# Performance work log

Hardware: AMD Instinct MI355X
Metric: run time of the kernel (lower is better)

The kernel has to match this reference:

```python
import jax, jax.numpy as jnp
import numpy as np

B, S, D, ENC_S = 4, 1024, 1024, 512
DI, DFF, DFE = 2048, 4096, 2048
NA, NB, E, H = 2, 6, 8, 16
TOP_K = 2


def setup_inputs():
    key = jax.random.key(0)
    ks = jax.random.split(key, 24)
    s = 0.02
    n = jax.random.normal
    return {
        "x": n(ks[0], (B, S, D), jnp.float32),
        "encoder_out": n(ks[1], (B, ENC_S, D), jnp.float32),
        "encoder_mask": jnp.ones((B, ENC_S), dtype=bool),
        "padding_mask": jnp.ones((B, S), dtype=bool),
        "encoder_available": jax.random.randint(ks[2], (B,), 0, 2, jnp.int32),
        "ln_g": jnp.ones((D,), jnp.float32),
        "ln_b": jnp.zeros((D,), jnp.float32),
        "ssm_Win": s * n(ks[3], (D, 2 * DI), jnp.float32),
        "ssm_a": n(ks[4], (DI,), jnp.float32),
        "ssm_Wout": s * n(ks[5], (DI, D), jnp.float32),
        "attn_Wqkv": s * n(ks[6], (D, 3 * D), jnp.float32),
        "attn_Wo": s * n(ks[7], (D, D), jnp.float32),
        "beta_ssm": 0.8 * jnp.ones((D,), jnp.float32),
        "beta_attn": 0.2 * jnp.ones((D,), jnp.float32),
        "se_W1": s * n(ks[8], (D, DFF), jnp.float32),
        "se_b1": jnp.zeros((DFF,), jnp.float32),
        "se_W2": s * n(ks[9], (DFF, D), jnp.float32),
        "se_b2": jnp.zeros((D,), jnp.float32),
        "r_W": s * n(ks[10], (D + 1, E), jnp.float32),
        "r_b": jnp.zeros((E,), jnp.float32),
        "ea_Wq": s * n(ks[11], (NA, D, D), jnp.float32),
        "ea_Wk": s * n(ks[12], (NA, D, D), jnp.float32),
        "ea_Wv": s * n(ks[13], (NA, D, D), jnp.float32),
        "ea_Wo": s * n(ks[14], (NA, D, D), jnp.float32),
        "ea_W1": s * n(ks[15], (NA, D, DFE), jnp.float32),
        "ea_W2": s * n(ks[16], (NA, DFE, D), jnp.float32),
        "eb_W1": s * n(ks[17], (NB, D, DFE), jnp.float32),
        "eb_W2": s * n(ks[18], (NB, DFE, D), jnp.float32),
    }


def _moe_forward(x, encoder_out, ln_g, ln_b, ssm_Win, ssm_a, ssm_Wout,
                 attn_Wqkv, attn_Wo, beta_ssm, beta_attn,
                 se_W1, se_b1, se_W2, se_b2, r_W, r_b,
                 ea_Wq, ea_Wk, ea_Wv, ea_Wo, ea_W1, ea_W2, eb_W1, eb_W2,
                 encoder_mask, padding_mask, encoder_available):
    # ---- Hymba fusion: LayerNorm -> SSM + causal attention, per-channel mix ----
    mu = x.mean(-1, keepdims=True)
    var = ((x - mu) ** 2).mean(-1, keepdims=True)
    h = (x - mu) * jax.lax.rsqrt(var + 1e-5) * ln_g + ln_b

    # SSM pathway: gated diagonal linear recurrence h_t = a*h_{t-1} + (1-a)*u_t
    u = h @ ssm_Win                       # (B,S,2*DI)
    z, xs = jnp.split(u, 2, axis=-1)
    a = jax.nn.sigmoid(ssm_a)             # (DI,)
    a_full = jnp.broadcast_to(a, xs.shape)
    b_in = (1.0 - a) * xs

    def comb(c1, c2):
        a1, b1 = c1
        a2, b2 = c2
        return a1 * a2, a2 * b1 + b2

    hs = jax.lax.associative_scan(comb, (a_full, b_in), axis=1)[1]
    ssm_out = (hs * jax.nn.silu(z)) @ ssm_Wout   # (B,S,D)

    # Attention pathway: causal MHA with key padding mask
    dh = D // H
    qkv = h @ attn_Wqkv
    q, k, v = jnp.split(qkv, 3, axis=-1)
    sp = lambda t: t.reshape(B, S, H, dh).transpose(0, 2, 1, 3)  # (B,H,S,dh)
    q, k, v = sp(q), sp(k), sp(v)
    scores = jnp.einsum('bhqd,bhkd->bhqk', q, k) / np.sqrt(dh).astype(np.float32)
    causal = jnp.tril(jnp.ones((S, S), dtype=bool))
    keymask = padding_mask[:, None, None, :]
    scores = jnp.where(causal[None, None] & keymask, scores, -1e9)
    p = jax.nn.softmax(scores, axis=-1)
    ao = jnp.einsum('bhqk,bhkd->bhqd', p, v).transpose(0, 2, 1, 3).reshape(B, S, D)
    attn_out = ao @ attn_Wo

    x = x + beta_ssm * ssm_out + beta_attn * attn_out  # residual after fusion

    # ---- MoE ----
    N = B * S
    x_flat = x.reshape(N, D)
    enc_avail_tok = jnp.repeat(encoder_available.astype(x.dtype), S)[:, None]  # (N,1)

    shared_delta = jax.nn.gelu(x_flat @ se_W1 + se_b1) @ se_W2 + se_b2

    # Router: top-k gating over softmax(logits)
    logits = jnp.concatenate([x_flat, enc_avail_tok], axis=-1) @ r_W + r_b  # (N,E)
    probs = jax.nn.softmax(logits, axis=-1)
    topv, topi = jax.lax.top_k(probs, TOP_K)
    gates = jnp.zeros_like(probs).at[jnp.arange(N)[:, None], topi].set(topv)
    gates = gates / (gates.sum(-1, keepdims=True) + 1e-9)

    # Hard S-mode gate: zero type-A experts where encoder unavailable, renormalize
    s_mode = enc_avail_tok == 0                       # (N,1)
    type_a = jnp.arange(E) < NA                       # (E,)
    gates = jnp.where(s_mode & type_a[None, :], 0.0, gates)
    gates = gates / (gates.sum(-1, keepdims=True) + 1e-6)

    # Type-A experts: per-token cross-attention to own batch's encoder, then FFN.
    # (dense over tokens; zero gates kill inactive tokens -> same math as sparse dispatch)
    qA = jnp.einsum('bsd,edf->ebsf', x, ea_Wq)
    kA = jnp.einsum('bmd,edf->ebmf', encoder_out, ea_Wk)
    vA = jnp.einsum('bmd,edf->ebmf', encoder_out, ea_Wv)
    sA = jnp.einsum('ebsf,ebmf->ebsm', qA, kA) / np.sqrt(D).astype(np.float32)
    sA = jnp.where(encoder_mask[None, :, None, :], sA, -1e9)
    pA = jax.nn.softmax(sA, axis=-1)
    ctx = jnp.einsum('ebsm,ebmf->ebsf', pA, vA)
    hA = x[None] + jnp.einsum('ebsf,efd->ebsd', ctx, ea_Wo)
    outA = jnp.einsum('ebsh,ehd->ebsd',
                      jax.nn.gelu(jnp.einsum('ebsd,edh->ebsh', hA, ea_W1)), ea_W2)
    outA = outA.reshape(NA, N, D)

    # Type-B experts: plain FFN on tokens
    outB = jnp.einsum('enh,ehd->end',
                      jax.nn.gelu(jnp.einsum('nd,edh->enh', x_flat, eb_W1)), eb_W2)

    out_all = jnp.concatenate([outA, outB], axis=0)   # (E,N,D)
    routed_delta = jnp.einsum('ne,end->nd', gates, out_all)

    return x + (shared_delta + routed_delta).reshape(B, S, D)


def reference(x, encoder_out, encoder_mask, padding_mask, encoder_available,
              ln_g, ln_b, ssm_Win, ssm_a, ssm_Wout, attn_Wqkv, attn_Wo,
              beta_ssm, beta_attn, se_W1, se_b1, se_W2, se_b2, r_W, r_b,
              ea_Wq, ea_Wk, ea_Wv, ea_Wo, ea_W1, ea_W2, eb_W1, eb_W2):
    return _moe_forward(x, encoder_out, ln_g, ln_b, ssm_Win, ssm_a, ssm_Wout,
                        attn_Wqkv, attn_Wo, beta_ssm, beta_attn,
                        se_W1, se_b1, se_W2, se_b2, r_W, r_b,
                        ea_Wq, ea_Wk, ea_Wv, ea_Wo, ea_W1, ea_W2, eb_W1, eb_W2,
                        encoder_mask, padding_mask, encoder_available)
```

## Files before the change

kernel.cpp:

```cpp
#include <hip/hip_runtime.h>
#include <hip/hip_bf16.h>
#include <math.h>

#define BB 4
#define SS 1024
#define DD 1024
#define ENCS 512
#define DI 2048
#define DFF 4096
#define DFE 2048
#define NA 2
#define NB 6
#define NE 8
#define NH 16
#define NTOK (BB*SS)
#define W1SZ ((long)DD*DFE)

typedef unsigned short u16;
typedef __bf16 bfrag __attribute__((ext_vector_type(8)));
typedef float  ffrag __attribute__((ext_vector_type(4)));

__device__ __forceinline__ float gelu_f(float x) {
    const float c = 0.7978845608028654f;
    float t = tanhf(c * (x + 0.044715f * x * x * x));
    return 0.5f * x * (1.f + t);
}

__device__ __forceinline__ u16 f2bf(float f) {
    unsigned u = __float_as_uint(f);
    u += 0x7fffu + ((u >> 16) & 1u);
    return (u16)(u >> 16);
}

__device__ __forceinline__ void split_bf(float v, u16& hi, u16& lo) {
    hi = f2bf(v);
    float hf = __uint_as_float((unsigned)hi << 16);
    lo = f2bf(v - hf);
}

typedef const __attribute__((address_space(1))) unsigned int* gas_t;
typedef __attribute__((address_space(3))) unsigned int* las_t;
__device__ __forceinline__ void gload16(const u16* g, u16* l) {
    __builtin_amdgcn_global_load_lds((gas_t)g, (las_t)l, 16, 0, 0);
}

__device__ __forceinline__ int flds(int row, int p) {
    return row * 64 + (((p ^ (row & 7)) & 7) << 3);
}

__global__ __launch_bounds__(256) void gemm_mfma(
    const u16* __restrict__ A, const u16* __restrict__ Bt,
    float* __restrict__ Cf, u16* __restrict__ Ch,
    int M, int N, int K,
    long sAb, long sBb, long sCb,
    const float* __restrict__ bias, const float* __restrict__ res,
    const float* __restrict__ rowscale, int rs_stride,
    int accum, int do_gelu)
{
    __shared__ u16 As[3][4096];
    __shared__ u16 Bs[3][4096];
    const int tid = threadIdx.x;
    const int w = tid >> 6, l = tid & 63;
    const int wm = w >> 1, wn = w & 1;
    const int bz = blockIdx.z;
    A  += (long)bz * sAb;
    Bt += (long)bz * sBb;
    const int m0 = blockIdx.y * 128, n0 = blockIdx.x * 128;

    const int c0 = 2 * w, c1 = c0 + 1;
    const int rl0 = c0 * 16 + (l >> 2), rl1 = c1 * 16 + (l >> 2);
    const int p = l & 3;
    const int gb0 = p ^ ((rl0 ^ (rl0 >> 2)) & 3);
    const int gb1 = p ^ ((rl1 ^ (rl1 >> 2)) & 3);
    const u16* gA0 = A  + (long)(m0 + rl0) * K + gb0 * 8;
    const u16* gA1 = A  + (long)(m0 + rl1) * K + gb1 * 8;
    const u16* gB0 = Bt + (long)(n0 + rl0) * K + gb0 * 8;
    const u16* gB1 = Bt + (long)(n0 + rl1) * K + gb1 * 8;
    const int d0 = c0 * 512, d1 = c1 * 512;

    const int q = l >> 4, fr = l & 15;
    int offA[4], offB[4];
    #pragma unroll
    for (int t = 0; t < 4; t++) {
        int ra = wm * 64 + t * 16 + fr;
        offA[t] = ra * 32 + (q ^ ((ra ^ (ra >> 2)) & 3)) * 8;
        int rb = wn * 64 + t * 16 + fr;
        offB[t] = rb * 32 + (q ^ ((rb ^ (rb >> 2)) & 3)) * 8;
    }

    ffrag acc[16];
    #pragma unroll
    for (int i = 0; i < 16; i++) acc[i] = (ffrag){0.f, 0.f, 0.f, 0.f};

    const int nsteps = K >> 5;
    #define STAGE1(bi, k0) do { \
        gload16(gA0 + (k0), &As[bi][d0]); \
        gload16(gA1 + (k0), &As[bi][d1]); \
        gload16(gB0 + (k0), &Bs[bi][d0]); \
        gload16(gB1 + (k0), &Bs[bi][d1]); } while (0)

    STAGE1(0, 0);
    STAGE1(1, 32);
    int cur = 0;
    for (int t = 0; t < nsteps; ++t) {
        int rem = nsteps - 1 - t;
        if (rem >= 2) {
            int nb = cur + 2; if (nb >= 3) nb -= 3;
            STAGE1(nb, (t + 2) << 5);
            asm volatile("s_waitcnt vmcnt(8)" ::: "memory");
        } else if (rem == 1) {
            asm volatile("s_waitcnt vmcnt(4)" ::: "memory");
        } else {
            asm volatile("s_waitcnt vmcnt(0)" ::: "memory");
        }
        __builtin_amdgcn_s_barrier();
        bfrag af[4], bf[4];
        #pragma unroll
        for (int i = 0; i < 4; i++) {
            af[i] = *(const bfrag*)(&As[cur][0] + offA[i]);
            bf[i] = *(const bfrag*)(&Bs[cur][0] + offB[i]);
        }
        #pragma unroll
        for (int mt = 0; mt < 4; mt++)
            #pragma unroll
            for (int nt = 0; nt < 4; nt++)
                acc[mt * 4 + nt] = __builtin_amdgcn_mfma_f32_16x16x32_bf16(
                    af[mt], bf[nt], acc[mt * 4 + nt], 0, 0, 0);
        __builtin_amdgcn_s_barrier();
        cur = (cur == 2) ? 0 : cur + 1;
    }
    #undef STAGE1

    const long cbase = (long)bz * sCb;
    #pragma unroll
    for (int mt = 0; mt < 4; mt++) {
        #pragma unroll
        for (int nt = 0; nt < 4; nt++) {
            ffrag v = acc[mt * 4 + nt];
            int col = n0 + wn * 64 + nt * 16 + fr;
            int row0 = m0 + wm * 64 + mt * 16 + q * 4;
            float bv = bias ? bias[col] : 0.f;
            #pragma unroll
            for (int j = 0; j < 4; j++) {
                int row = row0 + j;
                float x = v[j] + bv;
                if (do_gelu) x = gelu_f(x);
                if (rowscale) x *= rowscale[(long)row * rs_stride];
                long idx = cbase + (long)row * N + col;
                if (res) x += res[(long)row * N + col];
                if (accum) { Cf[idx] += x; }
                else {
                    if (Cf) Cf[idx] = x;
                    if (Ch) Ch[idx] = f2bf(x);
                }
            }
        }
    }
}

__global__ __launch_bounds__(256) void gemm3_mfma(
    const u16* __restrict__ Ahi, const u16* __restrict__ Alo,
    const u16* __restrict__ Bhi, const u16* __restrict__ Blo,
    float* __restrict__ Cf, int M, int N, int K)
{
    __shared__ u16 Ah[2][4096];
    __shared__ u16 Al[2][4096];
    __shared__ u16 Bh[2][4096];
    __shared__ u16 Bl[2][4096];
    const int tid = threadIdx.x;
    const int w = tid >> 6, l = tid & 63;
    const int wm = w >> 1, wn = w & 1;
    const int m0 = blockIdx.y * 128, n0 = blockIdx.x * 128;

    const int c0 = 2 * w, c1 = c0 + 1;
    const int rl0 = c0 * 16 + (l >> 2), rl1 = c1 * 16 + (l >> 2);
    const int p = l & 3;
    const int gb0 = p ^ ((rl0 ^ (rl0 >> 2)) & 3);
    const int gb1 = p ^ ((rl1 ^ (rl1 >> 2)) & 3);
    const long oa0 = (long)(m0 + rl0) * K + gb0 * 8;
    const long oa1 = (long)(m0 + rl1) * K + gb1 * 8;
    const long ob0 = (long)(n0 + rl0) * K + gb0 * 8;
    const long ob1 = (long)(n0 + rl1) * K + gb1 * 8;
    const u16* gAh0 = Ahi + oa0; const u16* gAh1 = Ahi + oa1;
    const u16* gAl0 = Alo + oa0; const u16* gAl1 = Alo + oa1;
    const u16* gBh0 = Bhi + ob0; const u16* gBh1 = Bhi + ob1;
    const u16* gBl0 = Blo + ob0; const u16* gBl1 = Blo + ob1;
    const int d0 = c0 * 512, d1 = c1 * 512;

    const int q = l >> 4, fr = l & 15;
    int offA[4], offB[4];
    #pragma unroll
    for (int t = 0; t < 4; t++) {
        int ra = wm * 64 + t * 16 + fr;
        offA[t] = ra * 32 + (q ^ ((ra ^ (ra >> 2)) & 3)) * 8;
        int rb = wn * 64 + t * 16 + fr;
        offB[t] = rb * 32 + (q ^ ((rb ^ (rb >> 2)) & 3)) * 8;
    }

    ffrag acc[16];
    #pragma unroll
    for (int i = 0; i < 16; i++) acc[i] = (ffrag){0.f, 0.f, 0.f, 0.f};

    const int nsteps = K >> 5;
    #define STAGE3(bi, k0) do { \
        gload16(gAh0 + (k0), &Ah[bi][d0]); \
        gload16(gAh1 + (k0), &Ah[bi][d1]); \
        gload16(gAl0 + (k0), &Al[bi][d0]); \
        gload16(gAl1 + (k0), &Al[bi][d1]); \
        gload16(gBh0 + (k0), &Bh[bi][d0]); \
        gload16(gBh1 + (k0), &Bh[bi][d1]); \
        gload16(gBl0 + (k0), &Bl[bi][d0]); \
        gload16(gBl1 + (k0), &Bl[bi][d1]); } while (0)

    int cur = 0;
    STAGE3(0, 0);
    for (int t = 0; t < nsteps; ++t) {
        if (t + 1 < nsteps) {
            STAGE3(cur ^ 1, (t + 1) << 5);
            asm volatile("s_waitcnt vmcnt(8)" ::: "memory");
        } else {
            asm volatile("s_waitcnt vmcnt(0)" ::: "memory");
        }
        __builtin_amdgcn_s_barrier();
        bfrag ah[4], al[4], bh[4], bl[4];
        #pragma unroll
        for (int i = 0; i < 4; i++) {
            ah[i] = *(const bfrag*)(&Ah[cur][0] + offA[i]);
            al[i] = *(const bfrag*)(&Al[cur][0] + offA[i]);
            bh[i] = *(const bfrag*)(&Bh[cur][0] + offB[i]);
            bl[i] = *(const bfrag*)(&Bl[cur][0] + offB[i]);
        }
        #pragma unroll
        for (int mt = 0; mt < 4; mt++) {
            #pragma unroll
            for (int nt = 0; nt < 4; nt++) {
                ffrag a = acc[mt * 4 + nt];
                a = __builtin_amdgcn_mfma_f32_16x16x32_bf16(ah[mt], bh[nt], a, 0, 0, 0);
                a = __builtin_amdgcn_mfma_f32_16x16x32_bf16(ah[mt], bl[nt], a, 0, 0, 0);
                a = __builtin_amdgcn_mfma_f32_16x16x32_bf16(al[mt], bh[nt], a, 0, 0, 0);
                acc[mt * 4 + nt] = a;
            }
        }
        __builtin_amdgcn_s_barrier();
        cur ^= 1;
    }
    #undef STAGE3

    #pragma unroll
    for (int mt = 0; mt < 4; mt++) {
        #pragma unroll
        for (int nt = 0; nt < 4; nt++) {
            ffrag v = acc[mt * 4 + nt];
            int col = n0 + wn * 64 + nt * 16 + fr;
            int row0 = m0 + wm * 64 + mt * 16 + q * 4;
            #pragma unroll
            for (int j = 0; j < 4; j++)
                Cf[(long)(row0 + j) * N + col] = v[j];
        }
    }
}

static inline void ggemm(hipStream_t st, const u16* A, const u16* Bt,
    float* Cf, u16* Ch, int M, int N, int K, int batch,
    long sA, long sB, long sC,
    const float* bias, const float* res, const float* rs, int rss,
    int accum, int gelu)
{
    dim3 g(N / 128, M / 128, batch), b(256);
    gemm_mfma<<<g, b, 0, st>>>(A, Bt, Cf, Ch, M, N, K, sA, sB, sC,
                               bias, res, rs, rss, accum, gelu);
}

static inline void ggemm3(hipStream_t st, const u16* Ahi, const u16* Alo,
    const u16* Bhi, const u16* Blo, float* Cf, int M, int N, int K)
{
    dim3 g(N / 128, M / 128, 1), b(256);
    gemm3_mfma<<<g, b, 0, st>>>(Ahi, Alo, Bhi, Blo, Cf, M, N, K);
}

__global__ __launch_bounds__(256) void moe_w1(
    const u16* __restrict__ Xa, const u16* __restrict__ Xb,
    const u16* __restrict__ W1a, const u16* __restrict__ W1b,
    u16* __restrict__ ffp,
    const int* __restrict__ idxAll, const int* __restrict__ cntAll,
    const int* __restrict__ offAll, int N, int K)
{
    const int z = blockIdx.z;
    const int m0 = blockIdx.y * 128;
    if (m0 >= cntAll[z]) return;
    const int* idx = idxAll + z * NTOK;
    const u16* X  = (z < NA) ? (Xa + (long)z * NTOK * DD) : Xb;
    const u16* Wt = (z < 4) ? (W1a + (long)z * W1SZ) : (W1b + (long)(z - 4) * W1SZ);
    u16* ff = ffp + (long)offAll[z] * N;

    __shared__ u16 As[3][4096];
    __shared__ u16 Bs[3][4096];
    const int tid = threadIdx.x;
    const int w = tid >> 6, l = tid & 63;
    const int wm = w >> 1, wn = w & 1;
    const int n0 = blockIdx.x * 128;
    const int c0 = 2 * w, c1 = c0 + 1;
    const int rl0 = c0 * 16 + (l >> 2), rl1 = c1 * 16 + (l >> 2);
    const int p = l & 3;
    const int gb0 = p ^ ((rl0 ^ (rl0 >> 2)) & 3);
    const int gb1 = p ^ ((rl1 ^ (rl1 >> 2)) & 3);
    const int t0 = idx[m0 + rl0], t1 = idx[m0 + rl1];
    const u16* gA0 = X + (long)t0 * K + gb0 * 8;
    const u16* gA1 = X + (long)t1 * K + gb1 * 8;
    const u16* gB0 = Wt + (long)(n0 + rl0) * K + gb0 * 8;
    const u16* gB1 = Wt + (long)(n0 + rl1) * K + gb1 * 8;
    const int d0 = c0 * 512, d1 = c1 * 512;
    const int q = l >> 4, fr = l & 15;
    int offA[4], offB[4];
    #pragma unroll
    for (int t = 0; t < 4; t++) {
        int ra = wm * 64 + t * 16 + fr;
        offA[t] = ra * 32 + (q ^ ((ra ^ (ra >> 2)) & 3)) * 8;
        int rb = wn * 64 + t * 16 + fr;
        offB[t] = rb * 32 + (q ^ ((rb ^ (rb >> 2)) & 3)) * 8;
    }
    ffrag acc[16];
    #pragma unroll
    for (int i = 0; i < 16; i++) acc[i] = (ffrag){0.f, 0.f, 0.f, 0.f};

    const int nsteps = K >> 5;
    #define STAGEM(bi, k0) do { \
        gload16(gA0 + (k0), &As[bi][d0]); \
        gload16(gA1 + (k0), &As[bi][d1]); \
        gload16(gB0 + (k0), &Bs[bi][d0]); \
        gload16(gB1 + (k0), &Bs[bi][d1]); } while (0)

    STAGEM(0, 0);
    STAGEM(1, 32);
    int cur = 0;
    for (int t = 0; t < nsteps; ++t) {
        int rem = nsteps - 1 - t;
        if (rem >= 2) {
            int nb = cur + 2; if (nb >= 3) nb -= 3;
            STAGEM(nb, (t + 2) << 5);
            asm volatile("s_waitcnt vmcnt(8)" ::: "memory");
        } else if (rem == 1) {
            asm volatile("s_waitcnt vmcnt(4)" ::: "memory");
        } else {
            asm volatile("s_waitcnt vmcnt(0)" ::: "memory");
        }
        __builtin_amdgcn_s_barrier();
        bfrag af[4], bf[4];
        #pragma unroll
        for (int i = 0; i < 4; i++) {
            af[i] = *(const bfrag*)(&As[cur][0] + offA[i]);
            bf[i] = *(const bfrag*)(&Bs[cur][0] + offB[i]);
        }
        #pragma unroll
        for (int mt = 0; mt < 4; mt++)
            #pragma unroll
            for (int nt = 0; nt < 4; nt++)
                acc[mt * 4 + nt] = __builtin_amdgcn_mfma_f32_16x16x32_bf16(
                    af[mt], bf[nt], acc[mt * 4 + nt], 0, 0, 0);
        __builtin_amdgcn_s_barrier();
        cur = (cur == 2) ? 0 : cur + 1;
    }
    #undef STAGEM

    #pragma unroll
    for (int mt = 0; mt < 4; mt++)
        #pragma unroll
        for (int nt = 0; nt < 4; nt++) {
            ffrag v = acc[mt * 4 + nt];
            int col = n0 + wn * 64 + nt * 16 + fr;
            int row0 = m0 + wm * 64 + mt * 16 + q * 4;
            #pragma unroll
            for (int j = 0; j < 4; j++)
                ff[(long)(row0 + j) * N + col] = f2bf(gelu_f(v[j]));
        }
}

__global__ __launch_bounds__(256) void moe_w2(
    const u16* __restrict__ ffp,
    const u16* __restrict__ W2a, const u16* __restrict__ W2b,
    float* __restrict__ out,
    const int* __restrict__ idxAll, const float* __restrict__ gvAll,
    const int* __restrict__ cntAll, const int* __restrict__ offAll,
    int N, int K)
{
    const int z = blockIdx.z;
    const int cnt = cntAll[z];
    const int m0 = blockIdx.y * 128;
    if (m0 >= cnt) return;
    const int* idx = idxAll + z * NTOK;
    const float* gval = gvAll + z * NTOK;
    const u16* Aseg = ffp + (long)offAll[z] * K;
    const u16* Wt = (z < 4) ? (W2a + (long)z * W1SZ) : (W2b + (long)(z - 4) * W1SZ);

    __shared__ u16 As[3][4096];
    __shared__ u16 Bs[3][4096];
    const int tid = threadIdx.x;
    const int w = tid >> 6, l = tid & 63;
    const int wm = w >> 1, wn = w & 1;
    const int n0 = blockIdx.x * 128;
    const int c0 = 2 * w, c1 = c0 + 1;
    const int rl0 = c0 * 16 + (l >> 2), rl1 = c1 * 16 + (l >> 2);
    const int p = l & 3;
    const int gb0 = p ^ ((rl0 ^ (rl0 >> 2)) & 3);
    const int gb1 = p ^ ((rl1 ^ (rl1 >> 2)) & 3);
    const u16* gA0 = Aseg + (long)(m0 + rl0) * K + gb0 * 8;
    const u16* gA1 = Aseg + (long)(m0 + rl1) * K + gb1 * 8;
    const u16* gB0 = Wt + (long)(n0 + rl0) * K + gb0 * 8;
    const u16* gB1 = Wt + (long)(n0 + rl1) * K + gb1 * 8;
    const int d0 = c0 * 512, d1 = c1 * 512;
    const int q = l >> 4, fr = l & 15;
    int offA[4], offB[4];
    #pragma unroll
    for (int t = 0; t < 4; t++) {
        int ra = wm * 64 + t * 16 + fr;
        offA[t] = ra * 32 + (q ^ ((ra ^ (ra >> 2)) & 3)) * 8;
        int rb = wn * 64 + t * 16 + fr;
        offB[t] = rb * 32 + (q ^ ((rb ^ (rb >> 2)) & 3)) * 8;
    }
    ffrag acc[16];
    #pragma unroll
    for (int i = 0; i < 16; i++) acc[i] = (ffrag){0.f, 0.f, 0.f, 0.f};

    const int nsteps = K >> 5;
    #define STAGEW(bi, k0) do { \
        gload16(gA0 + (k0), &As[bi][d0]); \
        gload16(gA1 + (k0), &As[bi][d1]); \
        gload16(gB0 + (k0), &Bs[bi][d0]); \
        gload16(gB1 + (k0), &Bs[bi][d1]); } while (0)

    STAGEW(0, 0);
    STAGEW(1, 32);
    int cur = 0;
    for (int t = 0; t < nsteps; ++t) {
        int rem = nsteps - 1 - t;
        if (rem >= 2) {
            int nb = cur + 2; if (nb >= 3) nb -= 3;
            STAGEW(nb, (t + 2) << 5);
            asm volatile("s_waitcnt vmcnt(8)" ::: "memory");
        } else if (rem == 1) {
            asm volatile("s_waitcnt vmcnt(4)" ::: "memory");
        } else {
            asm volatile("s_waitcnt vmcnt(0)" ::: "memory");
        }
        __builtin_amdgcn_s_barrier();
        bfrag af[4], bf[4];
        #pragma unroll
        for (int i = 0; i < 4; i++) {
            af[i] = *(const bfrag*)(&As[cur][0] + offA[i]);
            bf[i] = *(const bfrag*)(&Bs[cur][0] + offB[i]);
        }
        #pragma unroll
        for (int mt = 0; mt < 4; mt++)
            #pragma unroll
            for (int nt = 0; nt < 4; nt++)
                acc[mt * 4 + nt] = __builtin_amdgcn_mfma_f32_16x16x32_bf16(
                    af[mt], bf[nt], acc[mt * 4 + nt], 0, 0, 0);
        __builtin_amdgcn_s_barrier();
        cur = (cur == 2) ? 0 : cur + 1;
    }
    #undef STAGEW

    #pragma unroll
    for (int mt = 0; mt < 4; mt++)
        #pragma unroll
        for (int nt = 0; nt < 4; nt++) {
            ffrag v = acc[mt * 4 + nt];
            int col = n0 + wn * 64 + nt * 16 + fr;
            int row0 = m0 + wm * 64 + mt * 16 + q * 4;
            #pragma unroll
            for (int j = 0; j < 4; j++) {
                int m = row0 + j;
                if (m < cnt)
                    atomicAdd(&out[(long)idx[m] * N + col], gval[m] * v[j]);
            }
        }
}

__global__ __launch_bounds__(256) void moe_zero(int* __restrict__ idx, int* __restrict__ cnt)
{
    int i = blockIdx.x * 256 + threadIdx.x;
    if (i < NE * NTOK) idx[i] = 0;
    if (i < NE) cnt[i] = 0;
}

__global__ __launch_bounds__(256) void moe_build(
    const float* __restrict__ gates, int* __restrict__ idx,
    float* __restrict__ gval, int* __restrict__ cnt)
{
    int t = blockIdx.x * 256 + threadIdx.x;
    #pragma unroll
    for (int e = 0; e < NE; e++) {
        float g = gates[(long)t * NE + e];
        if (g > 0.f) {
            int ppos = atomicAdd(&cnt[e], 1);
            idx[e * NTOK + ppos] = t;
            gval[e * NTOK + ppos] = g;
        }
    }
}

__global__ __launch_bounds__(64) void moe_off(
    const int* __restrict__ cnt, int* __restrict__ off)
{
    if (threadIdx.x == 0) {
        int o = 0;
        for (int e = 0; e < NE; e++) { off[e] = o; o += (cnt[e] + 127) & ~127; }
    }
}

__global__ __launch_bounds__(256) void convT_kernel(
    const float* __restrict__ src, u16* __restrict__ dst, int K, int N,
    long sS, long sD)
{
    __shared__ float t[32][33];
    src += (long)blockIdx.z * sS;
    dst += (long)blockIdx.z * sD;
    int n0 = blockIdx.x * 32, k0 = blockIdx.y * 32;
    int tx = threadIdx.x & 31, ty = threadIdx.x >> 5;
    #pragma unroll
    for (int j = 0; j < 4; j++)
        t[ty + j * 8][tx] = src[(long)(k0 + ty + j * 8) * N + n0 + tx];
    __syncthreads();
    #pragma unroll
    for (int j = 0; j < 4; j++)
        dst[(long)(n0 + ty + j * 8) * K + k0 + tx] = f2bf(t[tx][ty + j * 8]);
}

__global__ __launch_bounds__(256) void convT2_kernel(
    const float* __restrict__ src, u16* __restrict__ dhi, u16* __restrict__ dlo,
    int K, int N)
{
    __shared__ float t[32][33];
    int n0 = blockIdx.x * 32, k0 = blockIdx.y * 32;
    int tx = threadIdx.x & 31, ty = threadIdx.x >> 5;
    #pragma unroll
    for (int j = 0; j < 4; j++)
        t[ty + j * 8][tx] = src[(long)(k0 + ty + j * 8) * N + n0 + tx];
    __syncthreads();
    #pragma unroll
    for (int j = 0; j < 4; j++) {
        float v = t[tx][ty + j * 8];
        u16 hi, lo; split_bf(v, hi, lo);
        long o = (long)(n0 + ty + j * 8) * K + k0 + tx;
        dhi[o] = hi; dlo[o] = lo;
    }
}

__global__ __launch_bounds__(256) void conv_kernel(
    const float* __restrict__ s, u16* __restrict__ d)
{
    int i = (blockIdx.x * 256 + threadIdx.x) * 4;
    float4 v = *(const float4*)(s + i);
    ushort4 o;
    o.x = f2bf(v.x); o.y = f2bf(v.y); o.z = f2bf(v.z); o.w = f2bf(v.w);
    *(ushort4*)(d + i) = o;
}

__global__ __launch_bounds__(256) void ln_kernel(
    const float* __restrict__ x, const float* __restrict__ g,
    const float* __restrict__ b, u16* __restrict__ hhi, u16* __restrict__ hlo)
{
    int token = blockIdx.x;
    int tid = threadIdx.x;
    const float* xr = x + (long)token * DD;
    float4 xv = *(const float4*)(xr + tid * 4);
    float s  = xv.x + xv.y + xv.z + xv.w;
    float sq = xv.x*xv.x + xv.y*xv.y + xv.z*xv.z + xv.w*xv.w;
    #pragma unroll
    for (int off = 32; off; off >>= 1) {
        s  += __shfl_xor(s, off);
        sq += __shfl_xor(sq, off);
    }
    __shared__ float ws[4], wq[4];
    int wid = tid >> 6, lane = tid & 63;
    if (lane == 0) { ws[wid] = s; wq[wid] = sq; }
    __syncthreads();
    s  = ws[0] + ws[1] + ws[2] + ws[3];
    sq = wq[0] + wq[1] + wq[2] + wq[3];
    float mu  = s * (1.f / DD);
    float var = sq * (1.f / DD) - mu * mu;
    float inv = rsqrtf(var + 1e-5f);
    float4 gv = *(const float4*)(g + tid * 4);
    float4 bv = *(const float4*)(b + tid * 4);
    float o[4];
    o[0] = (xv.x - mu) * inv * gv.x + bv.x;
    o[1] = (xv.y - mu) * inv * gv.y + bv.y;
    o[2] = (xv.z - mu) * inv * gv.z + bv.z;
    o[3] = (xv.w - mu) * inv * gv.w + bv.w;
    ushort4 oh, ol;
    split_bf(o[0], oh.x, ol.x); split_bf(o[1], oh.y, ol.y);
    split_bf(o[2], oh.z, ol.z); split_bf(o[3], oh.w, ol.w);
    *(ushort4*)(hhi + (long)token * DD + tid * 4) = oh;
    *(ushort4*)(hlo + (long)token * DD + tid * 4) = ol;
}

__global__ __launch_bounds__(256) void scan_p1(
    const float* __restrict__ u, const float* __restrict__ ssma,
    float* __restrict__ part)
{
    int i = blockIdx.x * 256 + threadIdx.x;
    int c = i & 2047, ch = (i >> 11) & 7, b = i >> 14;
    float a = 1.f / (1.f + expf(-ssma[c])), om = 1.f - a;
    const float* ux = u + (long)b * SS * (2 * DI) + DI + c;
    float h = 0.f;
    int t0 = ch * 128;
    #pragma unroll 4
    for (int t = t0; t < t0 + 128; ++t) h = a * h + om * ux[(long)t * (2 * DI)];
    part[i] = h;
}

__global__ __launch_bounds__(256) void scan_p2(
    const float* __restrict__ ssma, const float* __restrict__ part,
    float* __restrict__ init)
{
    int j = blockIdx.x * 256 + threadIdx.x;
    int c = j & 2047, b = j >> 11;
    float a = 1.f / (1.f + expf(-ssma[c]));
    float ap = a;
    #pragma unroll
    for (int i = 0; i < 7; i++) ap *= ap;
    float carry = 0.f;
    int base = b * 16384 + c;
    #pragma unroll
    for (int ch = 0; ch < 8; ch++) {
        init[base + ch * 2048] = carry;
        carry = ap * carry + part[base + ch * 2048];
    }
}

__global__ __launch_bounds__(256) void scan_p3(
    const float* __restrict__ u, const float* __restrict__ ssma,
    const float* __restrict__ init,
    u16* __restrict__ ihi, u16* __restrict__ ilo)
{
    int i = blockIdx.x * 256 + threadIdx.x;
    int c = i & 2047, ch = (i >> 11) & 7, b = i >> 14;
    float a = 1.f / (1.f + expf(-ssma[c])), om = 1.f - a;
    const float* uz = u + (long)b * SS * (2 * DI) + c;
    long obase = (long)b * SS * DI + c;
    float h = init[i];
    int t0 = ch * 128;
    #pragma unroll 2
    for (int t = t0; t < t0 + 128; ++t) {
        float z  = uz[(long)t * (2 * DI)];
        float xv = uz[(long)t * (2 * DI) + DI];
        h = a * h + om * xv;
        float sz = z / (1.f + expf(-z));
        u16 hi, lo; split_bf(h * sz, hi, lo);
        ihi[obase + (long)t * DI] = hi;
        ilo[obase + (long)t * DI] = lo;
    }
}

__global__ __launch_bounds__(256) void qk_prep(
    const float* __restrict__ qkv,
    u16* __restrict__ Qhi, u16* __restrict__ Qlo,
    u16* __restrict__ Khi, u16* __restrict__ Klo)
{
    int tok = blockIdx.x * 4 + (threadIdx.x >> 6);
    int l = threadIdx.x & 63;
    int b = tok >> 10, s = tok & 1023;
    const float* src = qkv + (long)tok * 3072;
    #pragma unroll
    for (int h = 0; h < 16; h++) {
        long dst = ((long)(b * 16 + h) * 1024 + s) * 64 + l;
        u16 hi, lo;
        split_bf(src[h * 64 + l], hi, lo);
        Qhi[dst] = hi; Qlo[dst] = lo;
        split_bf(src[1024 + h * 64 + l], hi, lo);
        Khi[dst] = hi; Klo[dst] = lo;
    }
}

__global__ __launch_bounds__(256) void v_prep(
    const float* __restrict__ qkv, u16* __restrict__ Vthi, u16* __restrict__ Vtlo)
{
    __shared__ float t[64][65];
    int st = blockIdx.x, bh = blockIdx.y;
    int b = bh >> 4, h = bh & 15;
    int tid = threadIdx.x;
    #pragma unroll
    for (int i = 0; i < 16; i++) {
        int e = tid + i * 256;
        int sl = e >> 6, d = e & 63;
        t[sl][d] = qkv[((long)(b * 1024 + st * 64 + sl)) * 3072 + 2048 + h * 64 + d];
    }
    __syncthreads();
    #pragma unroll
    for (int i = 0; i < 16; i++) {
        int e = tid + i * 256;
        int d = e >> 6, sl = e & 63;
        float v = t[sl][d];
        u16 hi, lo; split_bf(v, hi, lo);
        long o = ((long)bh * 64 + d) * 1024 + st * 64 + sl;
        Vthi[o] = hi; Vtlo[o] = lo;
    }
}

__global__ __launch_bounds__(256) void flash_mfma(
    const u16* __restrict__ Qhi, const u16* __restrict__ Qlo,
    const u16* __restrict__ Khi, const u16* __restrict__ Klo,
    const u16* __restrict__ Vthi, const u16* __restrict__ Vtlo,
    u16* __restrict__ aohi, u16* __restrict__ aolo)
{
    __shared__ u16 Qh[4096], Ql[4096], Kh[4096], Kl[4096], Vh[4096], Vl[4096];
    __shared__ u16 Ph[4][1024], Pl[4][1024];
    const int qt = (SS / 64 - 1) - blockIdx.x, bh = blockIdx.y;
    const int tid = threadIdx.x, w = tid >> 6, l = tid & 63;
    const int q0 = qt * 64;
    const int lr = l >> 3, ps = l & 7;
    const int cg = l & 15, quad = l >> 4;

    #pragma unroll
    for (int cc = 0; cc < 2; cc++) {
        int c = 2 * w + cc;
        int r = c * 8 + lr;
        int pl = ps ^ (r & 7);
        long gq = ((long)bh * 1024 + q0 + r) * 64 + pl * 8;
        long gk = ((long)bh * 1024 + r) * 64 + pl * 8;
        long gv = ((long)bh * 64 + r) * 1024 + pl * 8;
        gload16(Qhi + gq, Qh + c * 512 + l * 8);
        gload16(Qlo + gq, Ql + c * 512 + l * 8);
        gload16(Khi + gk, Kh + c * 512 + l * 8);
        gload16(Klo + gk, Kl + c * 512 + l * 8);
        gload16(Vthi + gv, Vh + c * 512 + l * 8);
        gload16(Vtlo + gv, Vl + c * 512 + l * 8);
    }
    __syncthreads();

    const int qrow = w * 16 + cg;
    const int offQ0 = flds(qrow, quad), offQ1 = flds(qrow, 4 + quad);
    bfrag qh0 = *(const bfrag*)(Qh + offQ0);
    bfrag qh1 = *(const bfrag*)(Qh + offQ1);
    bfrag ql0 = *(const bfrag*)(Ql + offQ0);
    bfrag ql1 = *(const bfrag*)(Ql + offQ1);

    ffrag O[4];
    #pragma unroll
    for (int i = 0; i < 4; i++) O[i] = (ffrag){0.f, 0.f, 0.f, 0.f};
    float mrun[4], lrun[4];
    #pragma unroll
    for (int j = 0; j < 4; j++) { mrun[j] = -1e30f; lrun[j] = 0.f; }

    for (int kt = 0; kt <= qt; kt++) {
        const bool pf = (kt < qt);
        uint4 rkh[2], rkl[2], rvh[2], rvl[2];
        if (pf) {
            int k0n = (kt + 1) * 64;
            #pragma unroll
            for (int cc = 0; cc < 2; cc++) {
                int c = 2 * w + cc;
                int r = c * 8 + lr;
                int pl = ps ^ (r & 7);
                long gk = ((long)bh * 1024 + k0n + r) * 64 + pl * 8;
                long gv = ((long)bh * 64 + r) * 1024 + k0n + pl * 8;
                rkh[cc] = *(const uint4*)(Khi + gk);
                rkl[cc] = *(const uint4*)(Klo + gk);
                rvh[cc] = *(const uint4*)(Vthi + gv);
                rvl[cc] = *(const uint4*)(Vtlo + gv);
            }
        }

        float s[4][4];
        #pragma unroll
        for (int nt = 0; nt < 4; nt++) {
            ffrag sc = (ffrag){0.f, 0.f, 0.f, 0.f};
            int kr = nt * 16 + cg;
            bfrag kh0 = *(const bfrag*)(Kh + flds(kr, quad));
            bfrag kh1 = *(const bfrag*)(Kh + flds(kr, 4 + quad));
            bfrag kl0 = *(const bfrag*)(Kl + flds(kr, quad));
            bfrag kl1 = *(const bfrag*)(Kl + flds(kr, 4 + quad));
            sc = __builtin_amdgcn_mfma_f32_16x16x32_bf16(qh0, kh0, sc, 0, 0, 0);
            sc = __builtin_amdgcn_mfma_f32_16x16x32_bf16(qh1, kh1, sc, 0, 0, 0);
            sc = __builtin_amdgcn_mfma_f32_16x16x32_bf16(qh0, kl0, sc, 0, 0, 0);
            sc = __builtin_amdgcn_mfma_f32_16x16x32_bf16(qh1, kl1, sc, 0, 0, 0);
            sc = __builtin_amdgcn_mfma_f32_16x16x32_bf16(ql0, kh0, sc, 0, 0, 0);
            sc = __builtin_amdgcn_mfma_f32_16x16x32_bf16(ql1, kh1, sc, 0, 0, 0);
            bool last = (kt == qt);
            #pragma unroll
            for (int j = 0; j < 4; j++) {
                float v = sc[j] * 0.125f;
                if (last && (nt * 16 + cg > w * 16 + quad * 4 + j)) v = -1e30f;
                s[nt][j] = v;
            }
        }
        #pragma unroll
        for (int j = 0; j < 4; j++) {
            float rm = fmaxf(fmaxf(s[0][j], s[1][j]), fmaxf(s[2][j], s[3][j]));
            rm = fmaxf(rm, __shfl_xor(rm, 1));
            rm = fmaxf(rm, __shfl_xor(rm, 2));
            rm = fmaxf(rm, __shfl_xor(rm, 4));
            rm = fmaxf(rm, __shfl_xor(rm, 8));
            float mn = fmaxf(mrun[j], rm);
            float alpha = __expf(mrun[j] - mn);
            float rs = 0.f;
            #pragma unroll
            for (int nt = 0; nt < 4; nt++) {
                float pv = __expf(s[nt][j] - mn);
                s[nt][j] = pv;
                rs += pv;
            }
            rs += __shfl_xor(rs, 1);
            rs += __shfl_xor(rs, 2);
            rs += __shfl_xor(rs, 4);
            rs += __shfl_xor(rs, 8);
            lrun[j] = lrun[j] * alpha + rs;
            mrun[j] = mn;
            #pragma unroll
            for (int ct = 0; ct < 4; ct++) O[ct][j] *= alpha;
        }
        #pragma unroll
        for (int nt = 0; nt < 4; nt++)
            #pragma unroll
            for (int j = 0; j < 4; j++) {
                int row = quad * 4 + j, col = nt * 16 + cg;
                int addr = row * 64 + (((col >> 3) ^ (row & 7)) << 3) + (col & 7);
                float pv = s[nt][j];
                u16 phv = f2bf(pv);
                float pf2 = __uint_as_float((unsigned)phv << 16);
                Ph[w][addr] = phv;
                Pl[w][addr] = f2bf(pv - pf2);
            }
        bfrag p0h = *(const bfrag*)(&Ph[w][0] + flds(cg, quad));
        bfrag p1h = *(const bfrag*)(&Ph[w][0] + flds(cg, 4 + quad));
        bfrag p0l = *(const bfrag*)(&Pl[w][0] + flds(cg, quad));
        bfrag p1l = *(const bfrag*)(&Pl[w][0] + flds(cg, 4 + quad));
        #pragma unroll
        for (int ct = 0; ct < 4; ct++) {
            int vr = ct * 16 + cg;
            bfrag vh0 = *(const bfrag*)(Vh + flds(vr, quad));
            bfrag vh1 = *(const bfrag*)(Vh + flds(vr, 4 + quad));
            bfrag vl0 = *(const bfrag*)(Vl + flds(vr, quad));
            bfrag vl1 = *(const bfrag*)(Vl + flds(vr, 4 + quad));
            O[ct] = __builtin_amdgcn_mfma_f32_16x16x32_bf16(p0h, vh0, O[ct], 0, 0, 0);
            O[ct] = __builtin_amdgcn_mfma_f32_16x16x32_bf16(p1h, vh1, O[ct], 0, 0, 0);
            O[ct] = __builtin_amdgcn_mfma_f32_16x16x32_bf16(p0h, vl0, O[ct], 0, 0, 0);
            O[ct] = __builtin_amdgcn_mfma_f32_16x16x32_bf16(p1h, vl1, O[ct], 0, 0, 0);
            O[ct] = __builtin_amdgcn_mfma_f32_16x16x32_bf16(p0l, vh0, O[ct], 0, 0, 0);
            O[ct] = __builtin_amdgcn_mfma_f32_16x16x32_bf16(p1l, vh1, O[ct], 0, 0, 0);
        }
        if (pf) {
            __syncthreads();
            #pragma unroll
            for (int cc = 0; cc < 2; cc++) {
                int c = 2 * w + cc;
                *(uint4*)(Kh + c * 512 + l * 8) = rkh[cc];
                *(uint4*)(Kl + c * 512 + l * 8) = rkl[cc];
                *(uint4*)(Vh + c * 512 + l * 8) = rvh[cc];
                *(uint4*)(Vl + c * 512 + l * 8) = rvl[cc];
            }
            __syncthreads();
        }
    }
    int b = bh >> 4, h = bh & 15;
    #pragma unroll
    for (int j = 0; j < 4; j++) {
        float inv = 1.f / lrun[j];
        int srow = q0 + w * 16 + quad * 4 + j;
        long base = ((long)(b * 1024 + srow)) * 1024 + h * 64 + cg;
        #pragma unroll
        for (int ct = 0; ct < 4; ct++) {
            float v = O[ct][j] * inv;
            u16 hi, lo; split_bf(v, hi, lo);
            aohi[base + ct * 16] = hi;
            aolo[base + ct * 16] = lo;
        }
    }
}

__global__ __launch_bounds__(256) void combine_kernel(
    const float* __restrict__ x, const float* __restrict__ ssm,
    const float* __restrict__ attn, const float* __restrict__ bs,
    const float* __restrict__ ba, float* __restrict__ x1, u16* __restrict__ x1h)
{
    int i = (blockIdx.x * 256 + threadIdx.x) * 4;
    int d = i & (DD - 1);
    float4 xv = *(const float4*)(x + i);
    float4 sv = *(const float4*)(ssm + i);
    float4 av = *(const float4*)(attn + i);
    float4 b1 = *(const float4*)(bs + d);
    float4 b2 = *(const float4*)(ba + d);
    float4 o;
    o.x = xv.x + b1.x * sv.x + b2.x * av.x;
    o.y = xv.y + b1.y * sv.y + b2.y * av.y;
    o.z = xv.z + b1.z * sv.z + b2.z * av.z;
    o.w = xv.w + b1.w * sv.w + b2.w * av.w;
    *(float4*)(x1 + i) = o;
    ushort4 oh;
    oh.x = f2bf(o.x); oh.y = f2bf(o.y); oh.z = f2bf(o.z); oh.w = f2bf(o.w);
    *(ushort4*)(x1h + i) = oh;
}

__global__ __launch_bounds__(256) void router_kernel(
    const float* __restrict__ x1, const int* __restrict__ enc_avail,
    const float* __restrict__ rW, const float* __restrict__ rb,
    float* __restrict__ gates)
{
    int token = blockIdx.x * 4 + (threadIdx.x >> 6);
    int lane = threadIdx.x & 63;
    int b = token >> 10;
    float acc[NE];
    #pragma unroll
    for (int e = 0; e < NE; e++) acc[e] = 0.f;
    const float* xrow = x1 + (long)token * DD;
    for (int d = lane; d < DD; d += 64) {
        float xv = xrow[d];
        const float* w = rW + (long)d * NE;
        #pragma unroll
        for (int e = 0; e < NE; e++) acc[e] += xv * w[e];
    }
    #pragma unroll
    for (int e = 0; e < NE; e++) {
        #pragma unroll
        for (int off = 32; off; off >>= 1) acc[e] += __shfl_xor(acc[e], off);
    }
    if (lane == 0) {
        int avail = enc_avail[b];
        float av = (float)avail;
        float lg[NE], pr[NE];
        #pragma unroll
        for (int e = 0; e < NE; e++) lg[e] = acc[e] + av * rW[(long)DD * NE + e] + rb[e];
        float mx = lg[0];
        #pragma unroll
        for (int e = 1; e < NE; e++) mx = fmaxf(mx, lg[e]);
        float sum = 0.f;
        #pragma unroll
        for (int e = 0; e < NE; e++) { pr[e] = expf(lg[e] - mx); sum += pr[e]; }
        float isum = 1.f / sum;
        #pragma unroll
        for (int e = 0; e < NE; e++) pr[e] *= isum;
        int i1 = 0;
        #pragma unroll
        for (int e = 1; e < NE; e++) if (pr[e] > pr[i1]) i1 = e;
        int i2 = (i1 == 0) ? 1 : 0;
        #pragma unroll
        for (int e = 0; e < NE; e++) if (e != i1 && pr[e] > pr[i2]) i2 = e;
        float g[NE];
        #pragma unroll
        for (int e = 0; e < NE; e++) g[e] = 0.f;
        g[i1] = pr[i1]; g[i2] = pr[i2];
        float s1 = g[i1] + g[i2] + 1e-9f;
        #pragma unroll
        for (int e = 0; e < NE; e++) g[e] /= s1;
        if (avail == 0) { g[0] = 0.f; g[1] = 0.f; }
        float s2 = 1e-6f;
        #pragma unroll
        for (int e = 0; e < NE; e++) s2 += g[e];
        float is2 = 1.f / s2;
        #pragma unroll
        for (int e = 0; e < NE; e++) gates[(long)token * NE + e] = g[e] * is2;
    }
}

__global__ __launch_bounds__(256) void softmax512_kernel(
    const float* __restrict__ sA, u16* __restrict__ pA, float scale)
{
    int row = blockIdx.x * 4 + (threadIdx.x >> 6);
    int lane = threadIdx.x & 63;
    const float* r = sA + (long)row * ENCS;
    u16* o = pA + (long)row * ENCS;
    float v[8];
    #pragma unroll
    for (int j = 0; j < 8; j++) v[j] = r[lane + j * 64] * scale;
    float mx = v[0];
    #pragma unroll
    for (int j = 1; j < 8; j++) mx = fmaxf(mx, v[j]);
    #pragma unroll
    for (int off = 32; off; off >>= 1) mx = fmaxf(mx, __shfl_xor(mx, off));
    float sum = 0.f;
    #pragma unroll
    for (int j = 0; j < 8; j++) { v[j] = __expf(v[j] - mx); sum += v[j]; }
    #pragma unroll
    for (int off = 32; off; off >>= 1) sum += __shfl_xor(sum, off);
    float inv = 1.f / sum;
    #pragma unroll
    for (int j = 0; j < 8; j++) o[lane + j * 64] = f2bf(v[j] * inv);
}

extern "C" void kernel_launch(void* const* d_in, const int* in_sizes, int n_in,
                              void* d_out, int out_size, void* d_ws, size_t ws_size,
                              hipStream_t stream) {
    const float* x    = (const float*)d_in[0];
    const float* enc  = (const float*)d_in[1];
    const int*   eav  = (const int*)d_in[4];
    const float* ln_g = (const float*)d_in[5];
    const float* ln_b = (const float*)d_in[6];
    const float* Win  = (const float*)d_in[7];
    const float* ssma = (const float*)d_in[8];
    const float* Wout = (const float*)d_in[9];
    const float* Wqkv = (const float*)d_in[10];
    const float* Wo   = (const float*)d_in[11];
    const float* bSsm = (const float*)d_in[12];
    const float* bAtt = (const float*)d_in[13];
    const float* seW1 = (const float*)d_in[14];
    const float* seb1 = (const float*)d_in[15];
    const float* seW2 = (const float*)d_in[16];
    const float* seb2 = (const float*)d_in[17];
    const float* rW   = (const float*)d_in[18];
    const float* rb   = (const float*)d_in[19];
    const float* eaWq = (const float*)d_in[20];
    const float* eaWk = (const float*)d_in[21];
    const float* eaWv = (const float*)d_in[22];
    const float* eaWo = (const float*)d_in[23];
    const float* eaW1 = (const float*)d_in[24];
    const float* eaW2 = (const float*)d_in[25];
    const float* ebW1 = (const float*)d_in[26];
    const float* ebW2 = (const float*)d_in[27];
    float* out = (float*)d_out;

    float* F = (float*)d_ws;
    float* f_big  = F;
    float* f_ssm  = F + 16777216;
    float* f_x1   = F + 20971520;
    float* f_part = F + 25165824;
    float* f_init = F + 25231360;
    float* f_gate = F + 25296896;
    u16* U = (u16*)(F + 25329664);
    u16* u_h_hi  = U;
    u16* u_h_lo  = U + 4194304;
    u16* u_in_hi = U + 8388608;
    u16* u_in_lo = U + 16777216;
    u16* u_ao_hi = U + 25165824;
    u16* u_ao_lo = U + 29360128;
    u16* u_wt    = U + 33554432;
    u16* u_wt_lo = U + 37748736;
    int*   moe_idx = (int*)(U + 41943040);
    float* moe_gv  = (float*)(moe_idx + NE * NTOK);
    int*   moe_cnt = (int*)(moe_gv + NE * NTOK);
    int*   moe_offp = moe_cnt + NE;

    float* f_u    = f_big;
    float* f_qkv  = f_big;
    float* f_attn = f_big + 12582912;
    u16*   u_ff   = (u16*)f_big;
    u16*   u_enc  = u_h_hi + 2097152;
    u16*   u_x1   = u_h_lo;
    u16* u_Qhi = u_h_hi, *u_Qlo = u_h_lo;
    u16* u_Khi = u_in_hi, *u_Klo = u_in_hi + 4194304;
    u16* u_Vthi = u_in_lo, *u_Vtlo = u_in_lo + 4194304;

    u16*   wq2   = u_wt;
    u16*   wk2   = u_wt_lo;
    u16*   wv2   = (u16*)f_ssm;
    u16*   wo2   = (u16*)f_ssm + 4194304;
    u16*   qA2   = u_ao_hi;
    u16*   kA2   = u_in_hi;
    u16*   vAt2  = u_in_hi + 4194304;
    float* sA2   = (float*)u_in_lo;
    u16*   ctx2  = u_in_lo;
    u16*   ffpool = (u16*)f_big;
    u16*   hA2   = (u16*)(f_big + 10485760);
    u16*   pA2   = (u16*)(f_big + 14680064);
    u16*   w1a   = u_ao_hi;
    u16*   w1b   = u_in_hi;
    u16*   w2a   = u_wt;
    u16*   w2b   = (u16*)f_ssm;

    #define CONVT(src, Kd, Nd)  convT_kernel <<<dim3((Nd)/32,(Kd)/32,1), dim3(256), 0, stream>>>(src, u_wt, Kd, Nd, 0, 0)
    #define CONVTB(src, dst, Kd, Nd, nb) convT_kernel<<<dim3((Nd)/32,(Kd)/32,(nb)), dim3(256), 0, stream>>>(src, dst, Kd, Nd, (long)(Kd)*(Nd), (long)(Kd)*(Nd))
    #define CONVT2(src, Kd, Nd) convT2_kernel<<<dim3((Nd)/32,(Kd)/32), dim3(256), 0, stream>>>(src, u_wt, u_wt_lo, Kd, Nd)

    ln_kernel<<<dim3(NTOK), dim3(256), 0, stream>>>(x, ln_g, ln_b, u_h_hi, u_h_lo);
    CONVT2(Win, DD, 2 * DI);
    ggemm3(stream, u_h_hi, u_h_lo, u_wt, u_wt_lo, f_u, NTOK, 2 * DI, DD);
    scan_p1<<<dim3(256), dim3(256), 0, stream>>>(f_u, ssma, f_part);
    scan_p2<<<dim3(32), dim3(256), 0, stream>>>(ssma, f_part, f_init);
    scan_p3<<<dim3(256), dim3(256), 0, stream>>>(f_u, ssma, f_init, u_in_hi, u_in_lo);
    CONVT2(Wout, DI, DD);
    ggemm3(stream, u_in_hi, u_in_lo, u_wt, u_wt_lo, f_ssm, NTOK, DD, DI);
    CONVT2(Wqkv, DD, 3 * DD);
    ggemm3(stream, u_h_hi, u_h_lo, u_wt, u_wt_lo, f_qkv, NTOK, 3 * DD, DD);
    qk_prep<<<dim3(NTOK / 4), dim3(256), 0, stream>>>(f_qkv, u_Qhi, u_Qlo, u_Khi, u_Klo);
    v_prep<<<dim3(SS / 64, BB * NH), dim3(256), 0, stream>>>(f_qkv, u_Vthi, u_Vtlo);
    flash_mfma<<<dim3(SS / 64, BB * NH), dim3(256), 0, stream>>>(
        u_Qhi, u_Qlo, u_Khi, u_Klo, u_Vthi, u_Vtlo, u_ao_hi, u_ao_lo);
    CONVT2(Wo, DD, DD);
    ggemm3(stream, u_ao_hi, u_ao_lo, u_wt, u_wt_lo, f_attn, NTOK, DD, DD);
    combine_kernel<<<dim3(NTOK * DD / 1024), dim3(256), 0, stream>>>(
        x, f_ssm, f_attn, bSsm, bAtt, f_x1, u_x1);
    router_kernel<<<dim3(NTOK / 4), dim3(256), 0, stream>>>(f_x1, eav, rW, rb, f_gate);
    moe_zero<<<dim3((NE * NTOK + 255) / 256), dim3(256), 0, stream>>>(moe_idx, moe_cnt);
    moe_build<<<dim3(NTOK / 256), dim3(256), 0, stream>>>(f_gate, moe_idx, moe_gv, moe_cnt);
    moe_off<<<dim3(1), dim3(64), 0, stream>>>(moe_cnt, moe_offp);
    CONVT(seW1, DD, DFF);
    ggemm(stream, u_x1, u_wt, nullptr, u_ff, NTOK, DFF, DD, 1, 0, 0, 0,
          seb1, nullptr, nullptr, 0, 0, 1);
    CONVT(seW2, DFF, DD);
    ggemm(stream, u_ff, u_wt, out, nullptr, NTOK, DD, DFF, 1, 0, 0, 0,
          seb2, f_x1, nullptr, 0, 0, 0);
    conv_kernel<<<dim3(BB * ENCS * DD / 1024), dim3(256), 0, stream>>>(enc, u_enc);

    CONVTB(eaWq, wq2, DD, DD, 2);
    CONVTB(eaWk, wk2, DD, DD, 2);
    CONVTB(eaWv, wv2, DD, DD, 2);
    CONVTB(eaWo, wo2, DD, DD, 2);
    ggemm(stream, u_x1, wq2, nullptr, qA2, NTOK, DD, DD, 2,
          0, (long)DD * DD, (long)NTOK * DD, nullptr, nullptr, nullptr, 0, 0, 0);
    ggemm(stream, u_enc, wk2, nullptr, kA2, BB * ENCS, DD, DD, 2,
          0, (long)DD * DD, (long)BB * ENCS * DD, nullptr, nullptr, nullptr, 0, 0, 0);
    for (int e = 0; e < NA; ++e)
        ggemm(stream, wv2 + (long)e * DD * DD, u_enc, nullptr,
              vAt2 + (long)e * 4 * DD * ENCS, DD, ENCS, DD, BB,
              0, (long)ENCS * DD, (long)DD * ENCS, nullptr, nullptr, nullptr, 0, 0, 0);
    ggemm(stream, qA2, kA2, sA2, nullptr, SS, ENCS, DD, 2 * BB,
          (long)SS * DD, (long)ENCS * DD, (long)SS * ENCS,
          nullptr, nullptr, nullptr, 0, 0, 0);
    softmax512_kernel<<<dim3(2 * NTOK / 4), dim3(256), 0, stream>>>(sA2, pA2, 0.03125f);
    ggemm(stream, pA2, vAt2, nullptr, ctx2, SS, DD, ENCS, 2 * BB,
          (long)SS * ENCS, (long)DD * ENCS, (long)SS * DD,
          nullptr, nullptr, nullptr, 0, 0, 0);
    ggemm(stream, ctx2, wo2, nullptr, hA2, NTOK, DD, DD, 2,
          (long)NTOK * DD, (long)DD * DD, (long)NTOK * DD,
          nullptr, f_x1, nullptr, 0, 0, 0);

    CONVTB(eaW1, w1a, DD, DFE, 2);
    CONVTB(ebW1, w1a + 2 * W1SZ, DD, DFE, 2);
    CONVTB(ebW1 + 2 * W1SZ, w1b, DD, DFE, 4);
    CONVTB(eaW2, w2a, DFE, DD, 2);
    CONVTB(ebW2, w2a + 2 * W1SZ, DFE, DD, 2);
    CONVTB(ebW2 + 2 * W1SZ, w2b, DFE, DD, 4);
    moe_w1<<<dim3(DFE / 128, NTOK / 128, NE), dim3(256), 0, stream>>>(
        hA2, u_x1, w1a, w1b, ffpool, moe_idx, moe_cnt, moe_offp, DFE, DD);
    moe_w2<<<dim3(DD / 128, NTOK / 128, NE), dim3(256), 0, stream>>>(
        ffpool, w2a, w2b, out, moe_idx, moe_gv, moe_cnt, moe_offp, DD, DFE);
    (void)in_sizes; (void)n_in; (void)out_size; (void)ws_size;
}
```

Baseline: 1.477 ms.

## Double-buffer K tiles and use direct global-to-LDS loads in flash attention

Replaces the register-staged K/V prefetch in the causal flash-attention kernel with direct global-to-LDS loads. K is double-buffered in shared memory, and V is loaded into its single buffer after the PV matmul, with manual vmcnt waits and raw s_barrier calls in place of __syncthreads. This removes register pressure and the extra LDS store pass, and lets K loads overlap compute. In exchange it adds 16 KB of LDS, which may lower occupancy, and it relies on careful manual waitcnt ordering, where a wrong count would be a correctness risk.

```diff
diff --git a/kernel.cpp b/kernel.cpp
--- a/kernel.cpp
+++ b/kernel.cpp
@@ -703,7 +703,9 @@
     const u16* __restrict__ Vthi, const u16* __restrict__ Vtlo,
     u16* __restrict__ aohi, u16* __restrict__ aolo)
 {
-    __shared__ u16 Qh[4096], Ql[4096], Kh[4096], Kl[4096], Vh[4096], Vl[4096];
+    __shared__ u16 Qh[4096], Ql[4096];
+    __shared__ u16 Kh[2][4096], Kl[2][4096];
+    __shared__ u16 Vh[4096], Vl[4096];
     __shared__ u16 Ph[4][1024], Pl[4][1024];
     const int qt = (SS / 64 - 1) - blockIdx.x, bh = blockIdx.y;
     const int tid = threadIdx.x, w = tid >> 6, l = tid & 63;
@@ -721,12 +723,13 @@
         long gv = ((long)bh * 64 + r) * 1024 + pl * 8;
         gload16(Qhi + gq, Qh + c * 512 + l * 8);
         gload16(Qlo + gq, Ql + c * 512 + l * 8);
-        gload16(Khi + gk, Kh + c * 512 + l * 8);
-        gload16(Klo + gk, Kl + c * 512 + l * 8);
+        gload16(Khi + gk, Kh[0] + c * 512 + l * 8);
+        gload16(Klo + gk, Kl[0] + c * 512 + l * 8);
         gload16(Vthi + gv, Vh + c * 512 + l * 8);
         gload16(Vtlo + gv, Vl + c * 512 + l * 8);
     }
-    __syncthreads();
+    asm volatile("s_waitcnt vmcnt(0)" ::: "memory");
+    __builtin_amdgcn_s_barrier();
 
     const int qrow = w * 16 + cg;
     const int offQ0 = flds(qrow, quad), offQ1 = flds(qrow, 4 + quad);
@@ -742,10 +745,9 @@
     #pragma unroll
     for (int j = 0; j < 4; j++) { mrun[j] = -1e30f; lrun[j] = 0.f; }
 
+    int cur = 0;
     for (int kt = 0; kt <= qt; kt++) {
-        const bool pf = (kt < qt);
-        uint4 rkh[2], rkl[2], rvh[2], rvl[2];
-        if (pf) {
+        if (kt < qt) {
             int k0n = (kt + 1) * 64;
             #pragma unroll
             for (int cc = 0; cc < 2; cc++) {
@@ -753,23 +755,26 @@
                 int r = c * 8 + lr;
                 int pl = ps ^ (r & 7);
                 long gk = ((long)bh * 1024 + k0n + r) * 64 + pl * 8;
-                long gv = ((long)bh * 64 + r) * 1024 + k0n + pl * 8;
-                rkh[cc] = *(const uint4*)(Khi + gk);
-                rkl[cc] = *(const uint4*)(Klo + gk);
-                rvh[cc] = *(const uint4*)(Vthi + gv);
-                rvl[cc] = *(const uint4*)(Vtlo + gv);
+                gload16(Khi + gk, Kh[cur ^ 1] + c * 512 + l * 8);
+                gload16(Klo + gk, Kl[cur ^ 1] + c * 512 + l * 8);
             }
-        }
-
+            asm volatile("s_waitcnt vmcnt(4)" ::: "memory");
+        } else {
+            asm volatile("s_waitcnt vmcnt(0)" ::: "memory");
+        }
+        __builtin_amdgcn_s_barrier();
+
+        const u16* KhC = Kh[cur];
+        const u16* KlC = Kl[cur];
         float s[4][4];
         #pragma unroll
         for (int nt = 0; nt < 4; nt++) {
             ffrag sc = (ffrag){0.f, 0.f, 0.f, 0.f};
             int kr = nt * 16 + cg;
-            bfrag kh0 = *(const bfrag*)(Kh + flds(kr, quad));
-            bfrag kh1 = *(const bfrag*)(Kh + flds(kr, 4 + quad));
-            bfrag kl0 = *(const bfrag*)(Kl + flds(kr, quad));
-            bfrag kl1 = *(const bfrag*)(Kl + flds(kr, 4 + quad));
+            bfrag kh0 = *(const bfrag*)(KhC + flds(kr, quad));
+            bfrag kh1 = *(const bfrag*)(KhC + flds(kr, 4 + quad));
+            bfrag kl0 = *(const bfrag*)(KlC + flds(kr, quad));
+            bfrag kl1 = *(const bfrag*)(KlC + flds(kr, 4 + quad));
             sc = __builtin_amdgcn_mfma_f32_16x16x32_bf16(qh0, kh0, sc, 0, 0, 0);
             sc = __builtin_amdgcn_mfma_f32_16x16x32_bf16(qh1, kh1, sc, 0, 0, 0);
             sc = __builtin_amdgcn_mfma_f32_16x16x32_bf16(qh0, kl0, sc, 0, 0, 0);
@@ -839,18 +844,20 @@
             O[ct] = __builtin_amdgcn_mfma_f32_16x16x32_bf16(p0l, vh0, O[ct], 0, 0, 0);
             O[ct] = __builtin_amdgcn_mfma_f32_16x16x32_bf16(p1l, vh1, O[ct], 0, 0, 0);
         }
-        if (pf) {
-            __syncthreads();
+        __builtin_amdgcn_s_barrier();
+        if (kt < qt) {
+            int k0n = (kt + 1) * 64;
             #pragma unroll
             for (int cc = 0; cc < 2; cc++) {
                 int c = 2 * w + cc;
-                *(uint4*)(Kh + c * 512 + l * 8) = rkh[cc];
-                *(uint4*)(Kl + c * 512 + l * 8) = rkl[cc];
-                *(uint4*)(Vh + c * 512 + l * 8) = rvh[cc];
-                *(uint4*)(Vl + c * 512 + l * 8) = rvl[cc];
+                int r = c * 8 + lr;
+                int pl = ps ^ (r & 7);
+                long gv = ((long)bh * 64 + r) * 1024 + k0n + pl * 8;
+                gload16(Vthi + gv, Vh + c * 512 + l * 8);
+                gload16(Vtlo + gv, Vl + c * 512 + l * 8);
             }
-            __syncthreads();
-        }
+        }
+        cur ^= 1;
     }
     int b = bh >> 4, h = bh & 15;
     #pragma unroll
```

After: 1.424 ms. 3.6% less time.
